# Optimization experiments

Hardware: AMD Instinct MI355X
Metric: run time of the kernel (lower is better)

Reference implementation:

```python
import jax, jax.numpy as jnp
import numpy as np

B, T, D = 8, 1024, 1024
H, HD, KVH, R = 16, 64, 4, 256   # heads, head_dim, kv_heads, kv_lora_rank
K = 31                            # depthwise conv kernel
FF = 4 * D
EPS = 1e-5


def _ln(x, g, b):
    m = jnp.mean(x, -1, keepdims=True)
    v = jnp.mean((x - m) ** 2, -1, keepdims=True)
    return (x - m) * jax.lax.rsqrt(v + EPS) * g + b


def _rope_tables(seq, dim):
    inv = 1.0 / (10000.0 ** (np.arange(0, dim, 2, dtype=np.float32) / dim))
    t = np.arange(seq, dtype=np.float32)
    f = np.einsum('i,j->ij', t, inv)
    emb = np.concatenate([f, f], -1)
    return jnp.asarray(np.cos(emb)), jnp.asarray(np.sin(emb))


def _rope(x, cos, sin):
    # x: [B, h, T, HD]; cos/sin: [T, HD]
    x1, x2 = jnp.split(x, 2, axis=-1)
    return x * cos + jnp.concatenate([-x2, x1], -1) * sin


def setup_inputs() -> dict:
    key = jax.random.key(0)
    ks = iter(jax.random.split(key, 48))
    def w(shape, s=0.02):
        return jax.random.normal(next(ks), shape, jnp.float32) * s
    d = {}
    d['x'] = jax.random.normal(next(ks), (B, T, D), jnp.float32)
    d['ff1_ng'] = jnp.ones(D); d['ff1_nb'] = jnp.zeros(D)
    d['ff1_w1'] = w((D, FF)); d['ff1_b1'] = jnp.zeros(FF)
    d['ff1_w2'] = w((FF, D)); d['ff1_b2'] = jnp.zeros(D)
    d['attn_ng'] = jnp.ones(D); d['attn_nb'] = jnp.zeros(D)
    d['wq'] = w((D, H * HD)); d['wkva'] = w((D, R + HD))
    d['kvn_g'] = jnp.ones(R); d['kvn_b'] = jnp.zeros(R)
    d['wkvb'] = w((R, KVH * HD * 2)); d['wo'] = w((H * HD, D))
    d['conv_ng'] = jnp.ones(D); d['conv_nb'] = jnp.zeros(D)
    d['pw1_w'] = w((D, 2 * D)); d['pw1_b'] = jnp.zeros(2 * D)
    d['dw_w'] = w((D, 1, K)); d['dw_b'] = jnp.zeros(D)
    d['bn_g'] = jnp.ones(D); d['bn_b'] = jnp.zeros(D)
    d['bn_rm'] = jnp.zeros(D); d['bn_rv'] = jnp.ones(D)
    d['pw2_w'] = w((D, D)); d['pw2_b'] = jnp.zeros(D)
    d['ff2_ng'] = jnp.ones(D); d['ff2_nb'] = jnp.zeros(D)
    d['ff2_w1'] = w((D, FF)); d['ff2_b1'] = jnp.zeros(FF)
    d['ff2_w2'] = w((FF, D)); d['ff2_b2'] = jnp.zeros(D)
    d['fin_g'] = jnp.ones(D); d['fin_b'] = jnp.zeros(D)
    return d


def _ffn(x, ng, nb, w1, b1, w2, b2):
    h = jax.nn.silu(_ln(x, ng, nb) @ w1 + b1)
    return h @ w2 + b2


def _rmla(x, ng, nb, wq, wkva, kvn_g, kvn_b, wkvb, wo):
    h = _ln(x, ng, nb)
    q = (h @ wq).reshape(B, T, H, HD).transpose(0, 2, 1, 3)
    kva = h @ wkva                                  # [B,T,R+HD]; k_pe part unused (as in source)
    lat = _ln(kva[..., :R], kvn_g, kvn_b)
    kv = lat @ wkvb
    k = kv[..., :KVH * HD].reshape(B, T, KVH, HD).transpose(0, 2, 1, 3)
    v = kv[..., KVH * HD:].reshape(B, T, KVH, HD).transpose(0, 2, 1, 3)
    cos, sin = _rope_tables(T, HD)
    q = _rope(q, cos, sin)
    k = _rope(k, cos, sin)
    g = H // KVH
    k = jnp.repeat(k, g, axis=1)
    v = jnp.repeat(v, g, axis=1)
    s = jnp.einsum('bhqd,bhkd->bhqk', q, k) * (HD ** -0.5)
    a = jax.nn.softmax(s.astype(jnp.float32), axis=-1).astype(q.dtype)
    o = jnp.einsum('bhqk,bhkd->bhqd', a, v)
    o = o.transpose(0, 2, 1, 3).reshape(B, T, H * HD)
    return o @ wo


def _convmod(x, ng, nb, pw1_w, pw1_b, dw_w, dw_b, bn_g, bn_b, bn_rm, bn_rv, pw2_w, pw2_b):
    h = _ln(x, ng, nb)
    h = h @ pw1_w + pw1_b                           # [B,T,2D]
    a, gate = jnp.split(h, 2, axis=-1)
    h = a * jax.nn.sigmoid(gate)                    # GLU over channels
    h = h.transpose(0, 2, 1)                        # [B,D,T]
    h = jax.lax.conv_general_dilated(h, dw_w, (1,), [(K // 2, K // 2)],
                                     dimension_numbers=('NCH', 'OIH', 'NCH'),
                                     feature_group_count=D) + dw_b[None, :, None]
    h = (h - bn_rm[None, :, None]) * jax.lax.rsqrt(bn_rv[None, :, None] + EPS)
    h = h * bn_g[None, :, None] + bn_b[None, :, None]
    h = jax.nn.silu(h)
    h = h.transpose(0, 2, 1)                        # [B,T,D]
    return h @ pw2_w + pw2_b


def reference(x, ff1_ng, ff1_nb, ff1_w1, ff1_b1, ff1_w2, ff1_b2,
              attn_ng, attn_nb, wq, wkva, kvn_g, kvn_b, wkvb, wo,
              conv_ng, conv_nb, pw1_w, pw1_b, dw_w, dw_b, bn_g, bn_b, bn_rm, bn_rv, pw2_w, pw2_b,
              ff2_ng, ff2_nb, ff2_w1, ff2_b1, ff2_w2, ff2_b2, fin_g, fin_b):
    # Conformer block (macaron): half-FF, RMLA attention, gated depthwise conv, half-FF, final LN
    x = x + 0.5 * _ffn(x, ff1_ng, ff1_nb, ff1_w1, ff1_b1, ff1_w2, ff1_b2)
    x = x + _rmla(x, attn_ng, attn_nb, wq, wkva, kvn_g, kvn_b, wkvb, wo)
    x = x + _convmod(x, conv_ng, conv_nb, pw1_w, pw1_b, dw_w, dw_b, bn_g, bn_b, bn_rm, bn_rv, pw2_w, pw2_b)
    x = x + 0.5 * _ffn(x, ff2_ng, ff2_nb, ff2_w1, ff2_b1, ff2_w2, ff2_b2)
    return _ln(x, fin_g, fin_b)
```

## Files before the change

### kernel.cpp

```cpp
#include <hip/hip_runtime.h>
#include <stdint.h>

typedef unsigned short u16;
using bf16x8 = __attribute__((ext_vector_type(8))) __bf16;
using f32x4  = __attribute__((ext_vector_type(4))) float;

__device__ __forceinline__ u16 f2bf(float f) {
    uint32_t u = __float_as_uint(f);
    u += 0x7fffu + ((u >> 16) & 1u);
    return (u16)(u >> 16);
}
__device__ __forceinline__ float bf2f(u16 u) {
    return __uint_as_float(((uint32_t)u) << 16);
}
__device__ __forceinline__ void gload16(const void* g, void* l) {
    __builtin_amdgcn_global_load_lds(
        (__attribute__((address_space(1))) void*)(uintptr_t)g,
        (__attribute__((address_space(3))) void*)(uintptr_t)l,
        16, 0, 0);
}

template <int OUTF32>
__global__ __launch_bounds__(256) void ln_kernel(const float* __restrict__ in,
                                                 const float* __restrict__ g,
                                                 const float* __restrict__ b,
                                                 void* __restrict__ out, int D) {
    const int row = blockIdx.x;
    const int tid = threadIdx.x;
    const float* x = in + (size_t)row * D;
    const int nv = D >> 8;
    float v[4];
    float s1 = 0.f, s2 = 0.f;
    for (int i = 0; i < nv; ++i) {
        float t = x[tid + (i << 8)];
        v[i] = t; s1 += t; s2 += t * t;
    }
    for (int o = 1; o < 64; o <<= 1) {
        s1 += __shfl_xor(s1, o, 64);
        s2 += __shfl_xor(s2, o, 64);
    }
    __shared__ float r1[4], r2[4];
    const int w = tid >> 6;
    if ((tid & 63) == 0) { r1[w] = s1; r2[w] = s2; }
    __syncthreads();
    s1 = r1[0] + r1[1] + r1[2] + r1[3];
    s2 = r2[0] + r2[1] + r2[2] + r2[3];
    const float mean = s1 / (float)D;
    const float var  = s2 / (float)D - mean * mean;
    const float inv  = rsqrtf(var + 1e-5f);
    for (int i = 0; i < nv; ++i) {
        int c = tid + (i << 8);
        float y = (v[i] - mean) * inv * g[c] + b[c];
        if (OUTF32) ((float*)out)[(size_t)row * D + c] = y;
        else        ((u16*)out)[(size_t)row * D + c] = f2bf(y);
    }
}

template <int GLUPERM>
__global__ __launch_bounds__(256) void wconvert_t(const float* __restrict__ W0,
                                                  u16* __restrict__ Wt0,
                                                  const float* __restrict__ W1,
                                                  u16* __restrict__ Wt1,
                                                  int K, int N, int ldw) {
    const float* W = blockIdx.z ? W1 : W0;
    u16* Wt = blockIdx.z ? Wt1 : Wt0;
    __shared__ float tile[32][33];
    const int k0 = blockIdx.x * 32, n0 = blockIdx.y * 32;
    const int tx = threadIdx.x & 31, ty = threadIdx.x >> 5;
    const int csrc = GLUPERM ? ((tx & 1) * 1024 + (n0 >> 1) + (tx >> 1)) : (n0 + tx);
    for (int i = 0; i < 4; ++i)
        tile[ty + i * 8][tx] = W[(size_t)(k0 + ty + i * 8) * ldw + csrc];
    __syncthreads();
    for (int i = 0; i < 4; ++i)
        Wt[(size_t)(n0 + ty + i * 8) * K + k0 + tx] = f2bf(tile[tx][ty + i * 8]);
}

template <int EPI>
__global__ __launch_bounds__(256, 2) void gemm128p(const u16* __restrict__ A,
                                                   const u16* __restrict__ Bt,
                                                   const float* __restrict__ bias,
                                                   const float* __restrict__ res,
                                                   float rscale,
                                                   void* __restrict__ outp,
                                                   const float* __restrict__ CT,
                                                   const float* __restrict__ ST,
                                                   int M, int N, int K, int nbx) {
    __shared__ u16 sA[2][128 * 64];
    __shared__ u16 sB[2][128 * 64];
    const int tid = threadIdx.x, lane = tid & 63, w = tid >> 6;
    const int wm = w >> 1, wn = w & 1;
    const int fr = lane & 15, fq = lane >> 4, frx = fr & 7;
    const int cpx = gridDim.x >> 3;
    const int lid = (blockIdx.x & 7) * cpx + (blockIdx.x >> 3);
    const int bn0 = (lid % nbx) * 128;
    const int bm0 = (lid / nbx) * 128;

    f32x4 acc[4][4] = {};

    const int lrow = lane >> 3;
    const int lslot = (lane & 7) ^ lrow;
    const u16* ga0 = A  + (size_t)(bm0 + w * 8 + lrow) * K + lslot * 8;
    const u16* gb0 = Bt + (size_t)(bn0 + w * 8 + lrow) * K + lslot * 8;
    const size_t rstep32 = (size_t)32 * K;
    const int NK = K >> 6;

#define STAGE(bufi, kt)                                                         \
    {                                                                           \
        _Pragma("unroll")                                                       \
        for (int i = 0; i < 4; ++i) {                                           \
            gload16(ga0 + (kt) + i * rstep32, &sA[bufi][w * 512 + i * 2048]);   \
            gload16(gb0 + (kt) + i * rstep32, &sB[bufi][w * 512 + i * 2048]);   \
        }                                                                       \
    }
#define SB() __builtin_amdgcn_sched_barrier(0)

    STAGE(0, 0)
    STAGE(1, 64)
    asm volatile("s_waitcnt vmcnt(8)" ::: "memory");
    SB();
    __builtin_amdgcn_s_barrier();

    for (int s = 0; s < NK; ++s) {
        const int buf = s & 1;
        bf16x8 afr[4], bfr[4], afr2[4], bfr2[4];
#pragma unroll
        for (int i = 0; i < 4; ++i) {
            afr[i] = *(const bf16x8*)(&sA[buf][(wm * 64 + i * 16 + fr) * 64 + ((fq ^ frx) << 3)]);
            bfr[i] = *(const bf16x8*)(&sB[buf][(wn * 64 + i * 16 + fr) * 64 + ((fq ^ frx) << 3)]);
        }
        asm volatile("s_waitcnt lgkmcnt(0)" ::: "memory");
        SB();
        __builtin_amdgcn_s_setprio(1);
#pragma unroll
        for (int mi = 0; mi < 4; ++mi)
#pragma unroll
            for (int ni = 0; ni < 4; ++ni)
                acc[mi][ni] = __builtin_amdgcn_mfma_f32_16x16x32_bf16(
                    bfr[ni], afr[mi], acc[mi][ni], 0, 0, 0);
        __builtin_amdgcn_s_setprio(0);
#pragma unroll
        for (int i = 0; i < 4; ++i) {
            afr2[i] = *(const bf16x8*)(&sA[buf][(wm * 64 + i * 16 + fr) * 64 + (((4 + fq) ^ frx) << 3)]);
            bfr2[i] = *(const bf16x8*)(&sB[buf][(wn * 64 + i * 16 + fr) * 64 + (((4 + fq) ^ frx) << 3)]);
        }
        asm volatile("s_waitcnt lgkmcnt(0)" ::: "memory");
        SB();
        __builtin_amdgcn_s_barrier();
        if (s + 2 < NK) STAGE(buf, (s + 2) << 6)
        SB();
        __builtin_amdgcn_s_setprio(1);
#pragma unroll
        for (int mi = 0; mi < 4; ++mi)
#pragma unroll
            for (int ni = 0; ni < 4; ++ni)
                acc[mi][ni] = __builtin_amdgcn_mfma_f32_16x16x32_bf16(
                    bfr2[ni], afr2[mi], acc[mi][ni], 0, 0, 0);
        __builtin_amdgcn_s_setprio(0);
        if (s + 2 < NK) { asm volatile("s_waitcnt vmcnt(8)" ::: "memory"); }
        else            { asm volatile("s_waitcnt vmcnt(0)" ::: "memory"); }
        SB();
        __builtin_amdgcn_s_barrier();
    }

#pragma unroll
    for (int mi = 0; mi < 4; ++mi) {
        const int m = bm0 + wm * 64 + mi * 16 + fr;
        if (EPI == 5 || EPI == 6) {
            const int t = m & 1023;
            const int colbase = bn0 + wn * 64;
            const bool dorope = (EPI == 5) || (colbase < 256);
            if (dorope) {
#pragma unroll
                for (int ni = 0; ni < 2; ++ni) {
                    const int j0 = ni * 16 + fq * 4;
                    const f32x4 c = *(const f32x4*)(CT + t * 32 + j0);
                    const f32x4 sn = *(const f32x4*)(ST + t * 32 + j0);
                    union { uint2 u2; u16 hh[4]; } o1, o2;
#pragma unroll
                    for (int r = 0; r < 4; ++r) {
                        const float x1 = acc[mi][ni][r];
                        const float x2 = acc[mi][ni + 2][r];
                        o1.hh[r] = f2bf((x1 * c[r] - x2 * sn[r]) * rscale);
                        o2.hh[r] = f2bf((x2 * c[r] + x1 * sn[r]) * rscale);
                    }
                    *(uint2*)((u16*)outp + (size_t)m * N + colbase + j0) = o1.u2;
                    *(uint2*)((u16*)outp + (size_t)m * N + colbase + j0 + 32) = o2.u2;
                }
            } else {
#pragma unroll
                for (int ni = 0; ni < 4; ++ni) {
                    const int n0 = colbase + ni * 16 + fq * 4;
                    union { uint2 u2; u16 hh[4]; } ok;
#pragma unroll
                    for (int r = 0; r < 4; ++r) ok.hh[r] = f2bf(acc[mi][ni][r]);
                    *(uint2*)((u16*)outp + (size_t)m * N + n0) = ok.u2;
                }
            }
            continue;
        }
#pragma unroll
        for (int ni = 0; ni < 4; ++ni) {
            const int n0 = bn0 + wn * 64 + ni * 16 + fq * 4;
            if (EPI == 0 || EPI == 1) {
                union { uint2 u2; u16 hh[4]; } ok;
#pragma unroll
                for (int r = 0; r < 4; ++r) {
                    float v = acc[mi][ni][r] + (bias ? bias[n0 + r] : 0.f);
                    if (EPI == 1) v = v / (1.f + __expf(-v));
                    ok.hh[r] = f2bf(v);
                }
                *(uint2*)((u16*)outp + (size_t)m * N + n0) = ok.u2;
            } else if (EPI == 2) {
                f32x4 v;
#pragma unroll
                for (int r = 0; r < 4; ++r)
                    v[r] = acc[mi][ni][r] + (bias ? bias[n0 + r] : 0.f);
                *(f32x4*)((float*)outp + (size_t)m * N + n0) = v;
            } else if (EPI == 3) {
                const f32x4 rv = *(const f32x4*)(res + (size_t)m * N + n0);
                f32x4 v;
#pragma unroll
                for (int r = 0; r < 4; ++r)
                    v[r] = rv[r] + rscale * (acc[mi][ni][r] + (bias ? bias[n0 + r] : 0.f));
                *(f32x4*)((float*)outp + (size_t)m * N + n0) = v;
            } else if (EPI == 4) {
                float vv[4];
#pragma unroll
                for (int r = 0; r < 4; ++r) {
                    const int n = n0 + r;
                    vv[r] = acc[mi][ni][r] + bias[((n & 1) << 10) + (n >> 1)];
                }
                union { uint32_t u; u16 hh[2]; } ok;
                ok.hh[0] = f2bf(vv[0] / (1.f + __expf(-vv[1])));
                ok.hh[1] = f2bf(vv[2] / (1.f + __expf(-vv[3])));
                *(uint32_t*)((u16*)outp + (size_t)m * (N >> 1) + (n0 >> 1)) = ok.u;
            }
        }
    }
#undef STAGE
#undef SB
}

__global__ __launch_bounds__(256) void rope_tables_kernel(float* __restrict__ ct,
                                                          float* __restrict__ st) {
    const int i = blockIdx.x * 256 + threadIdx.x;
    const int t = i >> 5, j = i & 31;
    const float inv = powf(10000.f, -(float)j / 32.f);
    const float f = (float)t * inv;
    ct[i] = cosf(f);
    st[i] = sinf(f);
}

__global__ __launch_bounds__(256) void vtranspose_kernel(const u16* __restrict__ KV,
                                                         u16* __restrict__ Vt) {
    __shared__ u16 tile[32][33];
    const int t0 = blockIdx.x * 32, h0 = blockIdx.y * 32;
    const int bk = blockIdx.z;
    const int b = bk >> 2, kh = bk & 3;
    const int tx = threadIdx.x & 31, ty = threadIdx.x >> 5;
    for (int i = 0; i < 4; ++i)
        tile[ty + i * 8][tx] =
            KV[(size_t)(b * 1024 + t0 + ty + i * 8) * 512 + 256 + kh * 64 + h0 + tx];
    __syncthreads();
    for (int i = 0; i < 4; ++i)
        Vt[((size_t)bk * 64 + h0 + ty + i * 8) * 1024 + t0 + tx] = tile[tx][ty + i * 8];
}

__global__ __launch_bounds__(256) void attn_kernel(const u16* __restrict__ Q,
                                                   const u16* __restrict__ KV,
                                                   const u16* __restrict__ Vt,
                                                   u16* __restrict__ O) {
    __shared__ __align__(16) u16 sK[2][64 * 64];
    __shared__ __align__(16) u16 sV[2][64 * 64];
    __shared__ __align__(16) u16 sP[4][16 * 64];
    const int tid = threadIdx.x, lane = tid & 63, w = tid >> 6;
    const int fr = lane & 15, fq = lane >> 4, frx = fr & 7;
    const int bk = blockIdx.x, b = bk >> 2, kh = bk & 3;
    const int h = kh * 4 + w;
    const int q0 = blockIdx.y * 16;
    const int qrow = b * 1024 + q0 + fr;

    const int srow = w * 16 + (lane >> 3);
    const int sslot = (lane & 7) ^ ((lane >> 3) & 7);
    const u16* gK = KV + (size_t)(b * 1024 + srow) * 512 + kh * 64 + sslot * 8;
    const u16* gV = Vt + (size_t)((b * 4 + kh) * 64 + srow) * 1024 + sslot * 8;
    u16* dK = (u16*)sK + w * 16 * 64;
    u16* dV = (u16*)sV + w * 16 * 64;

    bf16x8 qf[2];
    qf[0] = *(const bf16x8*)(Q + (size_t)qrow * 1024 + h * 64 + fq * 8);
    qf[1] = *(const bf16x8*)(Q + (size_t)qrow * 1024 + h * 64 + 32 + fq * 8);

    f32x4 oacc[4] = {};
    float mrun = -1e30f, lrun = 0.f;
    u16* sPw = sP[w];

    gload16(gK, dK);
    gload16(gK + (size_t)8 * 512, dK + 8 * 64);
    gload16(gV, dV);
    gload16(gV + (size_t)8 * 1024, dV + 8 * 64);
    __syncthreads();

    int cur = 0;
    for (int t = 0; t < 16; ++t) {
        const int kv0 = t * 64;
        if (t < 15) {
            const int kn = kv0 + 64;
            const int nx = (cur ^ 1) * 4096;
            gload16(gK + (size_t)kn * 512,       dK + nx);
            gload16(gK + (size_t)(kn + 8) * 512, dK + nx + 8 * 64);
            gload16(gV + kn,                     dV + nx);
            gload16(gV + kn + (size_t)8 * 1024,  dV + nx + 8 * 64);
        }
        const u16* sKc = (u16*)sK + cur * 4096;
        const u16* sVc = (u16*)sV + cur * 4096;
        f32x4 sacc[4] = {};
#pragma unroll
        for (int ks = 0; ks < 2; ++ks)
#pragma unroll
            for (int nb = 0; nb < 4; ++nb) {
                const bf16x8 kf = *(const bf16x8*)(
                    sKc + (nb * 16 + fr) * 64 + (((ks * 4 + fq) ^ frx) << 3));
                sacc[nb] = __builtin_amdgcn_mfma_f32_16x16x32_bf16(kf, qf[ks], sacc[nb], 0, 0, 0);
            }
        float pm;
        {
            float a0 = fmaxf(fmaxf(sacc[0][0], sacc[0][1]), fmaxf(sacc[0][2], sacc[0][3]));
            float a1 = fmaxf(fmaxf(sacc[1][0], sacc[1][1]), fmaxf(sacc[1][2], sacc[1][3]));
            float a2 = fmaxf(fmaxf(sacc[2][0], sacc[2][1]), fmaxf(sacc[2][2], sacc[2][3]));
            float a3 = fmaxf(fmaxf(sacc[3][0], sacc[3][1]), fmaxf(sacc[3][2], sacc[3][3]));
            pm = fmaxf(fmaxf(a0, a1), fmaxf(a2, a3));
        }
        pm = fmaxf(pm, __shfl_xor(pm, 16, 64));
        pm = fmaxf(pm, __shfl_xor(pm, 32, 64));
        if (!__all(pm <= mrun + 8.f)) {
            const float mn = fmaxf(mrun, pm);
            const float al = __expf(mrun - mn);
            mrun = mn;
            lrun *= al;
#pragma unroll
            for (int f = 0; f < 4; ++f) {
                f32x4 tt = oacc[f];
#pragma unroll
                for (int r = 0; r < 4; ++r) tt[r] *= al;
                oacc[f] = tt;
            }
        }
        float rs = 0.f;
#pragma unroll
        for (int nb = 0; nb < 4; ++nb) {
            union { uint2 u2; u16 hh[4]; } pk;
#pragma unroll
            for (int r = 0; r < 4; ++r) {
                const float p = __expf(sacc[nb][r] - mrun);
                rs += p;
                pk.hh[r] = f2bf(p);
            }
            const int slotl = nb * 2 + (fq >> 1);
            *(uint2*)(sPw + fr * 64 + (((slotl ^ frx) << 3) | ((fq & 1) << 2))) = pk.u2;
        }
        rs += __shfl_xor(rs, 16, 64);
        rs += __shfl_xor(rs, 32, 64);
        lrun += rs;
        asm volatile("s_waitcnt lgkmcnt(0)" ::: "memory");
        __builtin_amdgcn_sched_barrier(0);
#pragma unroll
        for (int ks2 = 0; ks2 < 2; ++ks2) {
            const bf16x8 pf = *(const bf16x8*)(
                sPw + fr * 64 + (((ks2 * 4 + fq) ^ frx) << 3));
#pragma unroll
            for (int f = 0; f < 4; ++f) {
                const bf16x8 vf = *(const bf16x8*)(
                    sVc + (f * 16 + fr) * 64 + (((ks2 * 4 + fq) ^ frx) << 3));
                oacc[f] = __builtin_amdgcn_mfma_f32_16x16x32_bf16(vf, pf, oacc[f], 0, 0, 0);
            }
        }
        __syncthreads();
        cur ^= 1;
    }

    const float linv = 1.f / lrun;
#pragma unroll
    for (int f = 0; f < 4; ++f) {
        union { uint2 u2; u16 hh[4]; } ok;
#pragma unroll
        for (int r = 0; r < 4; ++r) ok.hh[r] = f2bf(oacc[f][r] * linv);
        *(uint2*)(O + (size_t)qrow * 1024 + h * 64 + f * 16 + fq * 4) = ok.u2;
    }
}

__global__ __launch_bounds__(256) void dwconv_kernel(const u16* __restrict__ G,
                                                     const float* __restrict__ wt,
                                                     const float* __restrict__ wb,
                                                     const float* __restrict__ bg,
                                                     const float* __restrict__ bb,
                                                     const float* __restrict__ rm,
                                                     const float* __restrict__ rv,
                                                     u16* __restrict__ out) {
    __shared__ u16 sg[38 * 256];
    const int tid = threadIdx.x;
    const int d = blockIdx.x * 256 + tid;
    const int t0 = blockIdx.y * 8;
    const int b = blockIdx.z;
    const size_t base = (size_t)b * 1024 * 1024 + d;
    for (int i = 0; i < 38; ++i) {
        const int t = t0 - 15 + i;
        sg[i * 256 + tid] = (t >= 0 && t < 1024) ? G[base + (size_t)t * 1024] : (u16)0;
    }
    __syncthreads();
    float wreg[31];
#pragma unroll
    for (int k = 0; k < 31; ++k) wreg[k] = wt[d * 31 + k];
    const float scale = bg[d] * rsqrtf(rv[d] + 1e-5f);
    const float addv = wb[d] - rm[d];
#pragma unroll
    for (int j = 0; j < 8; ++j) {
        float acc = 0.f;
#pragma unroll
        for (int k = 0; k < 31; ++k) acc += bf2f(sg[(j + k) * 256 + tid]) * wreg[k];
        float y = (acc + addv) * scale + bb[d];
        y = y / (1.f + __expf(-y));
        out[base + (size_t)(t0 + j) * 1024] = f2bf(y);
    }
}

extern "C" void kernel_launch(void* const* d_in, const int* in_sizes, int n_in,
                              void* d_out, int out_size, void* d_ws, size_t ws_size,
                              hipStream_t stream) {
    (void)in_sizes; (void)n_in; (void)out_size;

    const float* x       = (const float*)d_in[0];
    const float* ff1_ng  = (const float*)d_in[1];
    const float* ff1_nb  = (const float*)d_in[2];
    const float* ff1_w1  = (const float*)d_in[3];
    const float* ff1_b1  = (const float*)d_in[4];
    const float* ff1_w2  = (const float*)d_in[5];
    const float* ff1_b2  = (const float*)d_in[6];
    const float* attn_ng = (const float*)d_in[7];
    const float* attn_nb = (const float*)d_in[8];
    const float* wq      = (const float*)d_in[9];
    const float* wkva    = (const float*)d_in[10];
    const float* kvn_g   = (const float*)d_in[11];
    const float* kvn_b   = (const float*)d_in[12];
    const float* wkvb    = (const float*)d_in[13];
    const float* wo      = (const float*)d_in[14];
    const float* conv_ng = (const float*)d_in[15];
    const float* conv_nb = (const float*)d_in[16];
    const float* pw1_w   = (const float*)d_in[17];
    const float* pw1_b   = (const float*)d_in[18];
    const float* dw_w    = (const float*)d_in[19];
    const float* dw_b    = (const float*)d_in[20];
    const float* bn_g    = (const float*)d_in[21];
    const float* bn_b    = (const float*)d_in[22];
    const float* bn_rm   = (const float*)d_in[23];
    const float* bn_rv   = (const float*)d_in[24];
    const float* pw2_w   = (const float*)d_in[25];
    const float* pw2_b   = (const float*)d_in[26];
    const float* ff2_ng  = (const float*)d_in[27];
    const float* ff2_nb  = (const float*)d_in[28];
    const float* ff2_w1  = (const float*)d_in[29];
    const float* ff2_b1  = (const float*)d_in[30];
    const float* ff2_w2  = (const float*)d_in[31];
    const float* ff2_b2  = (const float*)d_in[32];
    const float* fin_g   = (const float*)d_in[33];
    const float* fin_b   = (const float*)d_in[34];

    const int M = 8192;
    char* ws = (char*)d_ws;
    size_t off = 0;
    auto alloc = [&](size_t bytes) {
        size_t o = off;
        off += (bytes + 255) & ~(size_t)255;
        return o;
    };
    const size_t o_ff1w1 = alloc((size_t)4096 * 1024 * 2);
    const size_t o_ff1w2 = alloc((size_t)1024 * 4096 * 2);
    const size_t o_wq    = alloc((size_t)1024 * 1024 * 2);
    const size_t o_wkva  = alloc((size_t)256 * 1024 * 2);
    const size_t o_wkvb  = alloc((size_t)512 * 256 * 2);
    const size_t o_wo    = alloc((size_t)1024 * 1024 * 2);
    const size_t o_pw1   = alloc((size_t)2048 * 1024 * 2);
    const size_t o_pw2   = alloc((size_t)1024 * 1024 * 2);
    const size_t o_ff2w1 = alloc((size_t)4096 * 1024 * 2);
    const size_t o_ff2w2 = alloc((size_t)1024 * 4096 * 2);
    const size_t o_ctab  = alloc((size_t)1024 * 32 * 4);
    const size_t o_stab  = alloc((size_t)1024 * 32 * 4);
    const size_t o_xres  = alloc((size_t)M * 1024 * 4);
    const size_t o_ln    = alloc((size_t)M * 1024 * 2);
    const size_t o_bufa  = alloc((size_t)64 * 1024 * 1024);
    if (ws_size < off) return;

    u16* BUFA = (u16*)(ws + o_bufa);
    u16* Qb    = BUFA;
    u16* KVb   = (u16*)((char*)BUFA + (16u << 20));
    float* KVA = (float*)((char*)BUFA + (24u << 20));
    u16* LAT   = (u16*)((char*)BUFA + (32u << 20));
    u16* VT    = (u16*)((char*)BUFA + (36u << 20));
    u16* OB    = (u16*)((char*)BUFA + (40u << 20));
    u16* PW1G  = BUFA;
    u16* CONVO = (u16*)((char*)BUFA + (16u << 20));
    u16* HID   = BUFA;

    u16* WT_FF1W1 = (u16*)(ws + o_ff1w1);
    u16* WT_FF1W2 = (u16*)(ws + o_ff1w2);
    u16* WT_WQ    = (u16*)(ws + o_wq);
    u16* WT_WKVA  = (u16*)(ws + o_wkva);
    u16* WT_WKVB  = (u16*)(ws + o_wkvb);
    u16* WT_WO    = (u16*)(ws + o_wo);
    u16* WT_PW1   = (u16*)(ws + o_pw1);
    u16* WT_PW2   = (u16*)(ws + o_pw2);
    u16* WT_FF2W1 = (u16*)(ws + o_ff2w1);
    u16* WT_FF2W2 = (u16*)(ws + o_ff2w2);
    float* CT = (float*)(ws + o_ctab);
    float* ST = (float*)(ws + o_stab);
    float* XR = (float*)(ws + o_xres);
    u16* LNB  = (u16*)(ws + o_ln);

    wconvert_t<0><<<dim3(32, 128, 2), 256, 0, stream>>>(ff1_w1, WT_FF1W1, ff2_w1, WT_FF2W1, 1024, 4096, 4096);
    wconvert_t<0><<<dim3(128, 32, 2), 256, 0, stream>>>(ff1_w2, WT_FF1W2, ff2_w2, WT_FF2W2, 4096, 1024, 1024);
    wconvert_t<0><<<dim3(32, 32, 2),  256, 0, stream>>>(wq, WT_WQ, wo, WT_WO, 1024, 1024, 1024);
    wconvert_t<0><<<dim3(32, 32, 1),  256, 0, stream>>>(pw2_w, WT_PW2, pw2_w, WT_PW2, 1024, 1024, 1024);
    wconvert_t<0><<<dim3(32, 8, 1),   256, 0, stream>>>(wkva, WT_WKVA, wkva, WT_WKVA, 1024, 256, 320);
    wconvert_t<0><<<dim3(8, 16, 1),   256, 0, stream>>>(wkvb, WT_WKVB, wkvb, WT_WKVB, 256, 512, 512);
    wconvert_t<1><<<dim3(32, 64, 1),  256, 0, stream>>>(pw1_w, WT_PW1, pw1_w, WT_PW1, 1024, 2048, 2048);
    rope_tables_kernel<<<128, 256, 0, stream>>>(CT, ST);

    ln_kernel<0><<<M, 256, 0, stream>>>(x, ff1_ng, ff1_nb, LNB, 1024);
    gemm128p<1><<<2048, 256, 0, stream>>>(LNB, WT_FF1W1, ff1_b1, nullptr, 0.f, HID, nullptr, nullptr, M, 4096, 1024, 32);
    gemm128p<3><<<512, 256, 0, stream>>>(HID, WT_FF1W2, ff1_b2, x, 0.5f, XR, nullptr, nullptr, M, 1024, 4096, 8);

    ln_kernel<0><<<M, 256, 0, stream>>>(XR, attn_ng, attn_nb, LNB, 1024);
    gemm128p<5><<<512, 256, 0, stream>>>(LNB, WT_WQ, nullptr, nullptr, 0.125f, Qb, CT, ST, M, 1024, 1024, 8);
    gemm128p<2><<<128, 256, 0, stream>>>(LNB, WT_WKVA, nullptr, nullptr, 0.f, KVA, nullptr, nullptr, M, 256, 1024, 2);
    ln_kernel<0><<<M, 256, 0, stream>>>(KVA, kvn_g, kvn_b, LAT, 256);
    gemm128p<6><<<256, 256, 0, stream>>>(LAT, WT_WKVB, nullptr, nullptr, 1.0f, KVb, CT, ST, M, 512, 256, 4);
    vtranspose_kernel<<<dim3(32, 2, 32), 256, 0, stream>>>(KVb, VT);
    attn_kernel<<<dim3(32, 64), 256, 0, stream>>>(Qb, KVb, VT, OB);
    gemm128p<3><<<512, 256, 0, stream>>>(OB, WT_WO, nullptr, XR, 1.f, XR, nullptr, nullptr, M, 1024, 1024, 8);

    ln_kernel<0><<<M, 256, 0, stream>>>(XR, conv_ng, conv_nb, LNB, 1024);
    gemm128p<4><<<1024, 256, 0, stream>>>(LNB, WT_PW1, pw1_b, nullptr, 0.f, PW1G, nullptr, nullptr, M, 2048, 1024, 16);
    dwconv_kernel<<<dim3(4, 128, 8), 256, 0, stream>>>(PW1G, dw_w, dw_b, bn_g, bn_b, bn_rm, bn_rv, CONVO);
    gemm128p<3><<<512, 256, 0, stream>>>(CONVO, WT_PW2, pw2_b, XR, 1.f, XR, nullptr, nullptr, M, 1024, 1024, 8);

    ln_kernel<0><<<M, 256, 0, stream>>>(XR, ff2_ng, ff2_nb, LNB, 1024);
    gemm128p<1><<<2048, 256, 0, stream>>>(LNB, WT_FF2W1, ff2_b1, nullptr, 0.f, HID, nullptr, nullptr, M, 4096, 1024, 32);
    gemm128p<3><<<512, 256, 0, stream>>>(HID, WT_FF2W2, ff2_b2, XR, 0.5f, XR, nullptr, nullptr, M, 1024, 4096, 8);

    ln_kernel<1><<<M, 256, 0, stream>>>(XR, fin_g, fin_b, d_out, 1024);
}
```

Measured before the change: 771.5 us.

## Add 256-row, 512-thread GEMM kernel for the large projection GEMMs

Adds a gemm256 kernel that uses 8 waves and 256xBN tiles (BN of 256 or 128, set by a template warp layout), with double-buffered LDS and direct global-to-LDS loads. The FFN, Q, output-projection and pointwise-conv GEMMs move to it. Larger tiles raise arithmetic intensity and cut global/L2 traffic per FLOP. In exchange the blocks use more LDS and registers, and there are fewer blocks per GEMM, which can hurt occupancy and the tail. The old gemm128p epilogue is trimmed to only the variants still launched with it.

```diff
diff --git a/kernel.cpp b/kernel.cpp
--- a/kernel.cpp
+++ b/kernel.cpp
@@ -73,6 +73,170 @@
     __syncthreads();
     for (int i = 0; i < 4; ++i)
         Wt[(size_t)(n0 + ty + i * 8) * K + k0 + tx] = f2bf(tile[tx][ty + i * 8]);
+}
+
+template <int EPI, int WM>
+__global__ __launch_bounds__(512, 2) void gemm256(const u16* __restrict__ A,
+                                                  const u16* __restrict__ Bt,
+                                                  const float* __restrict__ bias,
+                                                  const float* __restrict__ res,
+                                                  float rscale,
+                                                  void* __restrict__ outp,
+                                                  const float* __restrict__ CT,
+                                                  const float* __restrict__ ST,
+                                                  int M, int N, int K, int nbx) {
+    constexpr int WN = 8 / WM;
+    constexpr int BN = WN * 64;
+    constexpr int FM = 16 / WM;
+    __shared__ u16 sA[2][256 * 64];
+    __shared__ u16 sB[2][BN * 64];
+    const int tid = threadIdx.x, lane = tid & 63, w = tid >> 6;
+    const int wm = w / WN, wn = w % WN;
+    const int fr = lane & 15, fq = lane >> 4, frx = fr & 7;
+    const int cpx = gridDim.x >> 3;
+    const int lid = (blockIdx.x & 7) * cpx + (blockIdx.x >> 3);
+    const int bn0 = (lid % nbx) * BN;
+    const int bm0 = (lid / nbx) * 256;
+
+    f32x4 acc[FM][4] = {};
+
+    const int lrow = lane >> 3;
+    const int lslot = (lane & 7) ^ (lrow & 7);
+    const u16* ga = A  + (size_t)(bm0 + w * 8 + lrow) * K + lslot * 8;
+    const u16* gb = Bt + (size_t)(bn0 + w * 8 + lrow) * K + lslot * 8;
+    const size_t rs64 = (size_t)64 * K;
+    const int lbase = w * 8 * 64;
+
+    const int NK = K >> 6;
+
+#define STAGE(bufi, kt)                                                        \
+    {                                                                          \
+        _Pragma("unroll")                                                      \
+        for (int i = 0; i < 4; ++i)                                            \
+            gload16(ga + (kt) + i * rs64, &sA[bufi][lbase + i * 4096]);        \
+        _Pragma("unroll")                                                      \
+        for (int i = 0; i < BN / 64; ++i)                                      \
+            gload16(gb + (kt) + i * rs64, &sB[bufi][lbase + i * 4096]);        \
+    }
+
+    STAGE(0, 0)
+    STAGE(1, 64)
+    if constexpr (WM == 2) asm volatile("s_waitcnt vmcnt(8)" ::: "memory");
+    else                   asm volatile("s_waitcnt vmcnt(6)" ::: "memory");
+    __builtin_amdgcn_sched_barrier(0);
+    __builtin_amdgcn_s_barrier();
+
+    const int arow0 = wm * (256 / WM) + fr;
+    const int brow0 = wn * 64 + fr;
+
+    for (int s = 0; s < NK; ++s) {
+        const int buf = s & 1;
+        bf16x8 afr[FM], bfr[4];
+#pragma unroll
+        for (int mi = 0; mi < FM; ++mi)
+            afr[mi] = *(const bf16x8*)(&sA[buf][(arow0 + mi * 16) * 64 + ((fq ^ frx) << 3)]);
+#pragma unroll
+        for (int ni = 0; ni < 4; ++ni)
+            bfr[ni] = *(const bf16x8*)(&sB[buf][(brow0 + ni * 16) * 64 + ((fq ^ frx) << 3)]);
+        asm volatile("s_waitcnt lgkmcnt(0)" ::: "memory");
+        __builtin_amdgcn_sched_barrier(0);
+        __builtin_amdgcn_s_setprio(1);
+#pragma unroll
+        for (int mi = 0; mi < FM; ++mi)
+#pragma unroll
+            for (int ni = 0; ni < 4; ++ni)
+                acc[mi][ni] = __builtin_amdgcn_mfma_f32_16x16x32_bf16(
+                    bfr[ni], afr[mi], acc[mi][ni], 0, 0, 0);
+        __builtin_amdgcn_s_setprio(0);
+#pragma unroll
+        for (int mi = 0; mi < FM; ++mi)
+            afr[mi] = *(const bf16x8*)(&sA[buf][(arow0 + mi * 16) * 64 + (((4 + fq) ^ frx) << 3)]);
+#pragma unroll
+        for (int ni = 0; ni < 4; ++ni)
+            bfr[ni] = *(const bf16x8*)(&sB[buf][(brow0 + ni * 16) * 64 + (((4 + fq) ^ frx) << 3)]);
+        asm volatile("s_waitcnt lgkmcnt(0)" ::: "memory");
+        __builtin_amdgcn_sched_barrier(0);
+        __builtin_amdgcn_s_barrier();
+        if (s + 2 < NK) {
+            STAGE(buf, (s + 2) << 6)
+        }
+        __builtin_amdgcn_sched_barrier(0);
+        __builtin_amdgcn_s_setprio(1);
+#pragma unroll
+        for (int mi = 0; mi < FM; ++mi)
+#pragma unroll
+            for (int ni = 0; ni < 4; ++ni)
+                acc[mi][ni] = __builtin_amdgcn_mfma_f32_16x16x32_bf16(
+                    bfr[ni], afr[mi], acc[mi][ni], 0, 0, 0);
+        __builtin_amdgcn_s_setprio(0);
+        if (s + 2 < NK) {
+            if constexpr (WM == 2) asm volatile("s_waitcnt vmcnt(8)" ::: "memory");
+            else                   asm volatile("s_waitcnt vmcnt(6)" ::: "memory");
+        } else {
+            asm volatile("s_waitcnt vmcnt(0)" ::: "memory");
+        }
+        __builtin_amdgcn_sched_barrier(0);
+        __builtin_amdgcn_s_barrier();
+    }
+
+#pragma unroll
+    for (int mi = 0; mi < FM; ++mi) {
+        const int m = bm0 + wm * (256 / WM) + mi * 16 + fr;
+        if (EPI == 5) {
+            const int tq = m & 1023;
+            const int colbase = bn0 + wn * 64;
+#pragma unroll
+            for (int ni = 0; ni < 2; ++ni) {
+                const int j0 = ni * 16 + fq * 4;
+                const f32x4 c = *(const f32x4*)(CT + tq * 32 + j0);
+                const f32x4 sn = *(const f32x4*)(ST + tq * 32 + j0);
+                union { uint2 u2; u16 hh[4]; } o1, o2;
+#pragma unroll
+                for (int r = 0; r < 4; ++r) {
+                    const float x1 = acc[mi][ni][r];
+                    const float x2 = acc[mi][ni + 2][r];
+                    o1.hh[r] = f2bf((x1 * c[r] - x2 * sn[r]) * rscale);
+                    o2.hh[r] = f2bf((x2 * c[r] + x1 * sn[r]) * rscale);
+                }
+                *(uint2*)((u16*)outp + (size_t)m * N + colbase + j0) = o1.u2;
+                *(uint2*)((u16*)outp + (size_t)m * N + colbase + j0 + 32) = o2.u2;
+            }
+            continue;
+        }
+#pragma unroll
+        for (int ni = 0; ni < 4; ++ni) {
+            const int n0 = bn0 + wn * 64 + ni * 16 + fq * 4;
+            if (EPI == 0 || EPI == 1) {
+                union { uint2 u2; u16 hh[4]; } ok;
+#pragma unroll
+                for (int r = 0; r < 4; ++r) {
+                    float v = acc[mi][ni][r] + (bias ? bias[n0 + r] : 0.f);
+                    if (EPI == 1) v = v / (1.f + __expf(-v));
+                    ok.hh[r] = f2bf(v);
+                }
+                *(uint2*)((u16*)outp + (size_t)m * N + n0) = ok.u2;
+            } else if (EPI == 3) {
+                const f32x4 rv = *(const f32x4*)(res + (size_t)m * N + n0);
+                f32x4 v;
+#pragma unroll
+                for (int r = 0; r < 4; ++r)
+                    v[r] = rv[r] + rscale * (acc[mi][ni][r] + (bias ? bias[n0 + r] : 0.f));
+                *(f32x4*)((float*)outp + (size_t)m * N + n0) = v;
+            } else if (EPI == 4) {
+                float vv[4];
+#pragma unroll
+                for (int r = 0; r < 4; ++r) {
+                    const int n = n0 + r;
+                    vv[r] = acc[mi][ni][r] + bias[((n & 1) << 10) + (n >> 1)];
+                }
+                union { uint32_t u; u16 hh[2]; } ok;
+                ok.hh[0] = f2bf(vv[0] / (1.f + __expf(-vv[1])));
+                ok.hh[1] = f2bf(vv[2] / (1.f + __expf(-vv[3])));
+                *(uint32_t*)((u16*)outp + (size_t)m * (N >> 1) + (n0 >> 1)) = ok.u;
+            }
+        }
+    }
+#undef STAGE
 }
 
 template <int EPI>
@@ -112,12 +276,11 @@
             gload16(gb0 + (kt) + i * rstep32, &sB[bufi][w * 512 + i * 2048]);   \
         }                                                                       \
     }
-#define SB() __builtin_amdgcn_sched_barrier(0)
 
     STAGE(0, 0)
     STAGE(1, 64)
     asm volatile("s_waitcnt vmcnt(8)" ::: "memory");
-    SB();
+    __builtin_amdgcn_sched_barrier(0);
     __builtin_amdgcn_s_barrier();
 
     for (int s = 0; s < NK; ++s) {
@@ -129,7 +292,7 @@
             bfr[i] = *(const bf16x8*)(&sB[buf][(wn * 64 + i * 16 + fr) * 64 + ((fq ^ frx) << 3)]);
         }
         asm volatile("s_waitcnt lgkmcnt(0)" ::: "memory");
-        SB();
+        __builtin_amdgcn_sched_barrier(0);
         __builtin_amdgcn_s_setprio(1);
 #pragma unroll
         for (int mi = 0; mi < 4; ++mi)
@@ -144,10 +307,10 @@
             bfr2[i] = *(const bf16x8*)(&sB[buf][(wn * 64 + i * 16 + fr) * 64 + (((4 + fq) ^ frx) << 3)]);
         }
         asm volatile("s_waitcnt lgkmcnt(0)" ::: "memory");
-        SB();
+        __builtin_amdgcn_sched_barrier(0);
         __builtin_amdgcn_s_barrier();
         if (s + 2 < NK) STAGE(buf, (s + 2) << 6)
-        SB();
+        __builtin_amdgcn_sched_barrier(0);
         __builtin_amdgcn_s_setprio(1);
 #pragma unroll
         for (int mi = 0; mi < 4; ++mi)
@@ -158,30 +321,29 @@
         __builtin_amdgcn_s_setprio(0);
         if (s + 2 < NK) { asm volatile("s_waitcnt vmcnt(8)" ::: "memory"); }
         else            { asm volatile("s_waitcnt vmcnt(0)" ::: "memory"); }
-        SB();
+        __builtin_amdgcn_sched_barrier(0);
         __builtin_amdgcn_s_barrier();
     }
 
 #pragma unroll
     for (int mi = 0; mi < 4; ++mi) {
         const int m = bm0 + wm * 64 + mi * 16 + fr;
-        if (EPI == 5 || EPI == 6) {
-            const int t = m & 1023;
+        if (EPI == 6) {
+            const int tq = m & 1023;
             const int colbase = bn0 + wn * 64;
-            const bool dorope = (EPI == 5) || (colbase < 256);
-            if (dorope) {
+            if (colbase < 256) {
 #pragma unroll
                 for (int ni = 0; ni < 2; ++ni) {
                     const int j0 = ni * 16 + fq * 4;
-                    const f32x4 c = *(const f32x4*)(CT + t * 32 + j0);
-                    const f32x4 sn = *(const f32x4*)(ST + t * 32 + j0);
+                    const f32x4 c = *(const f32x4*)(CT + tq * 32 + j0);
+                    const f32x4 sn = *(const f32x4*)(ST + tq * 32 + j0);
                     union { uint2 u2; u16 hh[4]; } o1, o2;
 #pragma unroll
                     for (int r = 0; r < 4; ++r) {
                         const float x1 = acc[mi][ni][r];
                         const float x2 = acc[mi][ni + 2][r];
-                        o1.hh[r] = f2bf((x1 * c[r] - x2 * sn[r]) * rscale);
-                        o2.hh[r] = f2bf((x2 * c[r] + x1 * sn[r]) * rscale);
+                        o1.hh[r] = f2bf(x1 * c[r] - x2 * sn[r]);
+                        o2.hh[r] = f2bf(x2 * c[r] + x1 * sn[r]);
                     }
                     *(uint2*)((u16*)outp + (size_t)m * N + colbase + j0) = o1.u2;
                     *(uint2*)((u16*)outp + (size_t)m * N + colbase + j0 + 32) = o2.u2;
@@ -201,44 +363,14 @@
 #pragma unroll
         for (int ni = 0; ni < 4; ++ni) {
             const int n0 = bn0 + wn * 64 + ni * 16 + fq * 4;
-            if (EPI == 0 || EPI == 1) {
-                union { uint2 u2; u16 hh[4]; } ok;
-#pragma unroll
-                for (int r = 0; r < 4; ++r) {
-                    float v = acc[mi][ni][r] + (bias ? bias[n0 + r] : 0.f);
-                    if (EPI == 1) v = v / (1.f + __expf(-v));
-                    ok.hh[r] = f2bf(v);
-                }
-                *(uint2*)((u16*)outp + (size_t)m * N + n0) = ok.u2;
-            } else if (EPI == 2) {
-                f32x4 v;
-#pragma unroll
-                for (int r = 0; r < 4; ++r)
-                    v[r] = acc[mi][ni][r] + (bias ? bias[n0 + r] : 0.f);
-                *(f32x4*)((float*)outp + (size_t)m * N + n0) = v;
-            } else if (EPI == 3) {
-                const f32x4 rv = *(const f32x4*)(res + (size_t)m * N + n0);
-                f32x4 v;
-#pragma unroll
-                for (int r = 0; r < 4; ++r)
-                    v[r] = rv[r] + rscale * (acc[mi][ni][r] + (bias ? bias[n0 + r] : 0.f));
-                *(f32x4*)((float*)outp + (size_t)m * N + n0) = v;
-            } else if (EPI == 4) {
-                float vv[4];
-#pragma unroll
-                for (int r = 0; r < 4; ++r) {
-                    const int n = n0 + r;
-                    vv[r] = acc[mi][ni][r] + bias[((n & 1) << 10) + (n >> 1)];
-                }
-                union { uint32_t u; u16 hh[2]; } ok;
-                ok.hh[0] = f2bf(vv[0] / (1.f + __expf(-vv[1])));
-                ok.hh[1] = f2bf(vv[2] / (1.f + __expf(-vv[3])));
-                *(uint32_t*)((u16*)outp + (size_t)m * (N >> 1) + (n0 >> 1)) = ok.u;
-            }
+            f32x4 v;
+#pragma unroll
+            for (int r = 0; r < 4; ++r)
+                v[r] = acc[mi][ni][r] + (bias ? bias[n0 + r] : 0.f);
+            *(f32x4*)((float*)outp + (size_t)m * N + n0) = v;
         }
     }
 #undef STAGE
-#undef SB
 }
 
 __global__ __launch_bounds__(256) void rope_tables_kernel(float* __restrict__ ct,
@@ -526,26 +658,26 @@
     rope_tables_kernel<<<128, 256, 0, stream>>>(CT, ST);
 
     ln_kernel<0><<<M, 256, 0, stream>>>(x, ff1_ng, ff1_nb, LNB, 1024);
-    gemm128p<1><<<2048, 256, 0, stream>>>(LNB, WT_FF1W1, ff1_b1, nullptr, 0.f, HID, nullptr, nullptr, M, 4096, 1024, 32);
-    gemm128p<3><<<512, 256, 0, stream>>>(HID, WT_FF1W2, ff1_b2, x, 0.5f, XR, nullptr, nullptr, M, 1024, 4096, 8);
+    gemm256<1, 2><<<512, 512, 0, stream>>>(LNB, WT_FF1W1, ff1_b1, nullptr, 0.f, HID, nullptr, nullptr, M, 4096, 1024, 16);
+    gemm256<3, 4><<<256, 512, 0, stream>>>(HID, WT_FF1W2, ff1_b2, x, 0.5f, XR, nullptr, nullptr, M, 1024, 4096, 8);
 
     ln_kernel<0><<<M, 256, 0, stream>>>(XR, attn_ng, attn_nb, LNB, 1024);
-    gemm128p<5><<<512, 256, 0, stream>>>(LNB, WT_WQ, nullptr, nullptr, 0.125f, Qb, CT, ST, M, 1024, 1024, 8);
+    gemm256<5, 4><<<256, 512, 0, stream>>>(LNB, WT_WQ, nullptr, nullptr, 0.125f, Qb, CT, ST, M, 1024, 1024, 8);
     gemm128p<2><<<128, 256, 0, stream>>>(LNB, WT_WKVA, nullptr, nullptr, 0.f, KVA, nullptr, nullptr, M, 256, 1024, 2);
     ln_kernel<0><<<M, 256, 0, stream>>>(KVA, kvn_g, kvn_b, LAT, 256);
     gemm128p<6><<<256, 256, 0, stream>>>(LAT, WT_WKVB, nullptr, nullptr, 1.0f, KVb, CT, ST, M, 512, 256, 4);
     vtranspose_kernel<<<dim3(32, 2, 32), 256, 0, stream>>>(KVb, VT);
     attn_kernel<<<dim3(32, 64), 256, 0, stream>>>(Qb, KVb, VT, OB);
-    gemm128p<3><<<512, 256, 0, stream>>>(OB, WT_WO, nullptr, XR, 1.f, XR, nullptr, nullptr, M, 1024, 1024, 8);
+    gemm256<3, 4><<<256, 512, 0, stream>>>(OB, WT_WO, nullptr, XR, 1.f, XR, nullptr, nullptr, M, 1024, 1024, 8);
 
     ln_kernel<0><<<M, 256, 0, stream>>>(XR, conv_ng, conv_nb, LNB, 1024);
-    gemm128p<4><<<1024, 256, 0, stream>>>(LNB, WT_PW1, pw1_b, nullptr, 0.f, PW1G, nullptr, nullptr, M, 2048, 1024, 16);
+    gemm256<4, 2><<<256, 512, 0, stream>>>(LNB, WT_PW1, pw1_b, nullptr, 0.f, PW1G, nullptr, nullptr, M, 2048, 1024, 8);
     dwconv_kernel<<<dim3(4, 128, 8), 256, 0, stream>>>(PW1G, dw_w, dw_b, bn_g, bn_b, bn_rm, bn_rv, CONVO);
-    gemm128p<3><<<512, 256, 0, stream>>>(CONVO, WT_PW2, pw2_b, XR, 1.f, XR, nullptr, nullptr, M, 1024, 1024, 8);
+    gemm256<3, 4><<<256, 512, 0, stream>>>(CONVO, WT_PW2, pw2_b, XR, 1.f, XR, nullptr, nullptr, M, 1024, 1024, 8);
 
     ln_kernel<0><<<M, 256, 0, stream>>>(XR, ff2_ng, ff2_nb, LNB, 1024);
-    gemm128p<1><<<2048, 256, 0, stream>>>(LNB, WT_FF2W1, ff2_b1, nullptr, 0.f, HID, nullptr, nullptr, M, 4096, 1024, 32);
-    gemm128p<3><<<512, 256, 0, stream>>>(HID, WT_FF2W2, ff2_b2, XR, 0.5f, XR, nullptr, nullptr, M, 1024, 4096, 8);
+    gemm256<1, 2><<<512, 512, 0, stream>>>(LNB, WT_FF2W1, ff2_b1, nullptr, 0.f, HID, nullptr, nullptr, M, 4096, 1024, 16);
+    gemm256<3, 4><<<256, 512, 0, stream>>>(HID, WT_FF2W2, ff2_b2, XR, 0.5f, XR, nullptr, nullptr, M, 1024, 4096, 8);
 
     ln_kernel<1><<<M, 256, 0, stream>>>(XR, fin_g, fin_b, d_out, 1024);
 }
```

New measurement: 731.5 us. 5.2% less time.
